# Kernel tuning notes

Hardware: AMD Instinct MI355X
Metric: run time of the kernel (lower is better)

Reference implementation:

```python
import jax, jax.numpy as jnp
import numpy as np

N, R, A, F = 6000, 5, 8, 128
K, O = 2, 128
RADIUS = 0.028
ROT_DELTA = 1


def _kernel_matrix(n_radial, n_angular, radius):
    # polar grid of kernel vertices -> cartesian, shape (R, A, 2)
    r = radius * (np.arange(1, n_radial + 1, dtype=np.float64) / n_radial)
    theta = 2.0 * np.pi * np.arange(n_angular, dtype=np.float64) / n_angular
    x = r[:, None] * np.cos(theta)[None, :]
    y = r[:, None] * np.sin(theta)[None, :]
    return np.stack([x, y], axis=-1)


def _interp_coefficients(n_radial, n_angular, radius):
    # Gaussian interpolation weights w(rho_a,theta_b,rho_c,theta_d), normalized,
    # reshaped to (R, A, R*A) as in _configure_patch_operator.
    kv = _kernel_matrix(n_radial, n_angular, radius)           # (R, A, 2)
    flat = kv.reshape(-1, 2)                                   # (R*A, 2)
    d2 = ((kv[:, :, None, :] - flat[None, None, :, :]) ** 2).sum(-1)  # (R, A, R*A)
    sigma = radius / n_radial
    w = np.exp(-d2 / (2.0 * sigma * sigma))
    w = w / w.sum(axis=-1, keepdims=True)
    return w.astype(np.float32)


def setup_inputs() -> dict:
    key = jax.random.key(0)
    k1, k2, k3, k4, k5 = jax.random.split(key, 5)
    mesh_signal = jax.random.normal(k1, (N, F), dtype=jnp.float32)
    # barycentric coords: channel 0 = vertex indices (stored as float), channel 1 = weights summing to 1
    idx = jax.random.randint(k2, (N, R, A, 3), 0, N).astype(jnp.float32)
    w = jax.random.uniform(k3, (N, R, A, 3), dtype=jnp.float32)
    w = w / w.sum(axis=-1, keepdims=True)
    bary_coordinates = jnp.stack([idx, w], axis=-1)            # (N, R, A, 3, 2)
    kernel_weights = jax.random.normal(k4, (R, A, K, O, F), dtype=jnp.float32) * 0.05
    bias = jax.random.normal(k5, (K, O), dtype=jnp.float32) * 0.05
    interp_coeffs = jnp.asarray(_interp_coefficients(R, A, RADIUS))  # (R, A, R*A)
    return {"mesh_signal": mesh_signal, "bary_coordinates": bary_coordinates,
            "kernel_weights": kernel_weights, "bias": bias, "interp_coeffs": interp_coeffs}


def reference(mesh_signal, bary_coordinates, kernel_weights, bias, interp_coeffs):
    # 1) gather + barycentric interpolation
    idx = bary_coordinates[..., 0].astype(jnp.int32)           # (N, R, A, 3)
    w = bary_coordinates[..., 1]                               # (N, R, A, 3)
    collected = mesh_signal[idx]                               # (N, R, A, 3, F)
    sig = jnp.sum(w[..., None] * collected, axis=-2)           # (N, R, A, F)
    # 2) patch operator: F_x @ I[a,b]
    flat = sig.reshape(-1, R * A, F)                           # (N, R*A, F)
    patched = jnp.einsum('nqf,raq->nraf', flat, interp_coeffs)  # (N, R, A, F)
    # 3) rotation-shifted fold (splits=1 -> single chunk; splits don't change math)
    outs = []
    for rot in range(0, A, ROT_DELTA):
        rolled = jnp.roll(patched, shift=rot, axis=2)          # (N, R, A, F)
        s = jnp.einsum('nraf,rakof->nko', rolled, kernel_weights) + (R * A) * bias  # (N, K, O)
        outs.append(jax.nn.relu(s).sum(axis=1))                # (N, O)
    return jnp.stack(outs, axis=1)                             # (N, n_rotations, O)
```

## Files before the change

### kernel.cpp

```cpp
#include <hip/hip_runtime.h>
#include <hip/hip_bf16.h>


#define N_PTS 6000
#define RR 5
#define AA 8
#define FF 128
#define OO 128
#define QQ 40
#define KD2 1280
#define SIG_BLOCKS 750
#define W2_BLOCKS 128
#define CCQ 0.70710678118654752f
#define RT2 1.41421356237309515f

#define AHS ((size_t)N_PTS * KD2)
#define BHS ((size_t)512 * KD2)

typedef __bf16 bf16_t;
typedef __bf16 bf16x2 __attribute__((ext_vector_type(2)));
typedef __bf16 bf16x8 __attribute__((ext_vector_type(8)));
typedef float f32x4 __attribute__((ext_vector_type(4)));

#define GLOAD_LDS16(g, l)                                              \
  __builtin_amdgcn_global_load_lds(                                    \
      (const __attribute__((address_space(1))) void*)(g),              \
      (__attribute__((address_space(3))) void*)(l), 16, 0, 0)

#define DFT8V(xx, c, X0, X4, Xr1, Xi1, Xr2, Xi2, Xr3, Xi3)             \
  {                                                                    \
    const float s0_ = xx[0][c] + xx[4][c], s1_ = xx[1][c] + xx[5][c];  \
    const float s2_ = xx[2][c] + xx[6][c], s3_ = xx[3][c] + xx[7][c];  \
    const float d0_ = xx[0][c] - xx[4][c], d1_ = xx[1][c] - xx[5][c];  \
    const float d2_ = xx[2][c] - xx[6][c], d3_ = xx[3][c] - xx[7][c];  \
    const float e_ = CCQ * (d1_ - d3_), o_ = CCQ * (d1_ + d3_);        \
    X0 = (s0_ + s2_) + (s1_ + s3_);                                    \
    X4 = (s0_ + s2_) - (s1_ + s3_);                                    \
    Xr2 = s0_ - s2_; Xi2 = s3_ - s1_;                                  \
    Xr1 = d0_ + e_;  Xi1 = -(o_ + d2_);                                \
    Xr3 = d0_ - e_;  Xi3 = d2_ - o_;                                   \
  }

#define PACKP(dst, P, Q)                                               \
  {                                                                    \
    bf16x8 pv_;                                                        \
    pv_[0] = (bf16_t)P[0]; pv_[1] = (bf16_t)Q[0];                      \
    pv_[2] = (bf16_t)P[1]; pv_[3] = (bf16_t)Q[1];                      \
    pv_[4] = (bf16_t)P[2]; pv_[5] = (bf16_t)Q[2];                      \
    pv_[6] = (bf16_t)P[3]; pv_[7] = (bf16_t)Q[3];                      \
    *(bf16x8*)(dst) = pv_;                                             \
  }

__global__ __launch_bounds__(256, 6) void prep_fft_kernel(
    const float* __restrict__ mesh, const float* __restrict__ bary,
    const float* __restrict__ kw, const float* __restrict__ interp,
    bf16_t* __restrict__ Ahat, bf16_t* __restrict__ Bhat) {
  __shared__ float sh[1920];
  const int bx = blockIdx.x;
  const int tid = threadIdx.x;

  if (bx < SIG_BLOCKS) {
    const int slot = tid >> 5;
    const int l = tid & 31;
    const int n = bx * 8 + slot;
    const float* bbase = bary + (size_t)bx * 8 * (QQ * 6);
    for (int i = tid; i < 1920; i += 256) sh[i] = bbase[i];
    __syncthreads();
    const float* bp = sh + slot * 240;
    bf16_t* an = Ahat + (size_t)n * KD2 + l * 8;
#pragma unroll
    for (int rho = 0; rho < RR; ++rho) {
      float x[8][4];
#pragma unroll
      for (int a = 0; a < 8; ++a) {
        const float* rec = bp + (rho * 8 + a) * 6;
        const float2 p0 = *(const float2*)(rec);
        const float2 p1 = *(const float2*)(rec + 2);
        const float2 p2 = *(const float2*)(rec + 4);
        const float4 v0 =
            *(const float4*)(mesh + (size_t)((int)p0.x) * FF + l * 4);
        const float4 v1 =
            *(const float4*)(mesh + (size_t)((int)p1.x) * FF + l * 4);
        const float4 v2 =
            *(const float4*)(mesh + (size_t)((int)p2.x) * FF + l * 4);
        x[a][0] = p0.y * v0.x + p1.y * v1.x + p2.y * v2.x;
        x[a][1] = p0.y * v0.y + p1.y * v1.y + p2.y * v2.y;
        x[a][2] = p0.y * v0.z + p1.y * v1.z + p2.y * v2.z;
        x[a][3] = p0.y * v0.w + p1.y * v1.w + p2.y * v2.w;
      }
      float X0[4], X4[4], Xr1[4], Xi1[4], Xr2[4], Xi2[4], Xr3[4], Xi3[4];
#pragma unroll
      for (int c = 0; c < 4; ++c)
        DFT8V(x, c, X0[c], X4[c], Xr1[c], Xi1[c], Xr2[c], Xi2[c], Xr3[c],
              Xi3[c]);
      bf16_t* dst = an + rho * 256;
      PACKP(dst, X0, X4);
      PACKP(dst + AHS, Xr1, Xi1);
      PACKP(dst + 2 * AHS, Xr2, Xi2);
      PACKP(dst + 3 * AHS, Xr3, Xi3);
    }
  } else {
    const int j = (bx - SIG_BLOCKS) * 2 + (tid >> 7);
    const int f = tid & 127;
    for (int i = tid; i < RR * AA * QQ; i += 256) sh[i] = interp[i];
    __syncthreads();
    const int o = (j >> 1) & 127;
    const int k = j & 1;
    float acc[QQ];
#pragma unroll
    for (int q = 0; q < QQ; ++q) acc[q] = 0.f;
    for (int r = 0; r < RR; ++r) {
      for (int a = 0; a < AA; ++a) {
        const float kv =
            kw[((size_t)((r * AA + a) * 2 + k) * OO + o) * FF + f];
        const float4* ip = (const float4*)(sh + (r * AA + a) * QQ);
#pragma unroll
        for (int q4 = 0; q4 < QQ / 4; ++q4) {
          const float4 w4 = ip[q4];
          acc[q4 * 4 + 0] += w4.x * kv;
          acc[q4 * 4 + 1] += w4.y * kv;
          acc[q4 * 4 + 2] += w4.z * kv;
          acc[q4 * 4 + 3] += w4.w * kv;
        }
      }
    }
    const float SC = 0.125f;
    bf16_t* b1p = Bhat + (size_t)j * KD2;
    bf16_t* b2p = Bhat + (size_t)(256 + j) * KD2;
#pragma unroll
    for (int rho = 0; rho < RR; ++rho) {
      float xx[8][1];
#pragma unroll
      for (int a = 0; a < 8; ++a) xx[a][0] = acc[rho * 8 + a];
      float Y0, Y4, Yr1, Yi1, Yr2, Yi2, Yr3, Yi3;
      DFT8V(xx, 0, Y0, Y4, Yr1, Yi1, Yr2, Yi2, Yr3, Yi3);
      const int off = rho * 256 + f * 2;
      bf16x2 w;
      w[0] = (bf16_t)(Y0 * SC);   w[1] = (bf16_t)0.f;
      *(bf16x2*)(b1p + off) = w;
      w[0] = (bf16_t)0.f;         w[1] = (bf16_t)(Y4 * SC);
      *(bf16x2*)(b2p + off) = w;
      w[0] = (bf16_t)(Yr1 * SC);  w[1] = (bf16_t)(Yi1 * SC);
      *(bf16x2*)(b1p + BHS + off) = w;
      w[0] = (bf16_t)(Yi1 * SC);  w[1] = (bf16_t)(-Yr1 * SC);
      *(bf16x2*)(b2p + BHS + off) = w;
      w[0] = (bf16_t)(Yr2 * SC);  w[1] = (bf16_t)(Yi2 * SC);
      *(bf16x2*)(b1p + 2 * BHS + off) = w;
      w[0] = (bf16_t)(Yi2 * SC);  w[1] = (bf16_t)(-Yr2 * SC);
      *(bf16x2*)(b2p + 2 * BHS + off) = w;
      w[0] = (bf16_t)(Yr3 * SC);  w[1] = (bf16_t)(Yi3 * SC);
      *(bf16x2*)(b1p + 3 * BHS + off) = w;
      w[0] = (bf16_t)(Yi3 * SC);  w[1] = (bf16_t)(-Yr3 * SC);
      *(bf16x2*)(b2p + 3 * BHS + off) = w;
    }
  }
}

__global__ __launch_bounds__(256, 3) void gemm_fused_fft_kernel(
    const bf16_t* __restrict__ Ahat, const bf16_t* __restrict__ Bhat,
    const float* __restrict__ bias, float* __restrict__ out) {
  const int L = blockIdx.x;
  const int xcd = L & 7;
  const int t = L >> 3;
  const int g = xcd + 8 * (t >> 4);
  const int jt = t & 15;
  const int m0 = g * 128;
  if (m0 >= N_PTS) return;
  const int j0 = jt * 16;

  __shared__ bf16_t As0[128 * 64];
  __shared__ bf16_t As1[128 * 64];
  __shared__ bf16_t Bs0[32 * 64];
  __shared__ bf16_t Bs1[32 * 64];
  const int tid = threadIdx.x;
  const int wave = tid >> 6;
  const int lane = tid & 63;
  const int quad = lane >> 4;
  const int tl = lane & 15;
  const int wm = wave * 32;
  const int srow = lane >> 3;
  const int sc = (lane & 7) ^ srow;

  const int crow = wave * 8;
  const int colbase = (crow < 16) ? (j0 + crow) : (256 + j0 + (crow - 16));
  const int gcol = colbase + srow;

  static const float CF[4][8] = {
      {1, 1, 1, 1, 1, 1, 1, 1},
      {2, RT2, 0, -RT2, -2, -RT2, 0, RT2},
      {2, 0, -2, 0, 2, 0, -2, 0},
      {2, -RT2, 0, RT2, -2, RT2, 0, -RT2}};
  static const float SF[4][8] = {
      {1, -1, 1, -1, 1, -1, 1, -1},
      {0, -RT2, -2, -RT2, 0, RT2, 2, RT2},
      {0, -2, 0, 2, 0, -2, 0, 2},
      {0, -RT2, 2, -RT2, 0, RT2, -2, RT2}};

  f32x4 oacc[8][2];
#pragma unroll
  for (int rot = 0; rot < 8; ++rot)
#pragma unroll
    for (int mm = 0; mm < 2; ++mm) oacc[rot][mm] = {0.f, 0.f, 0.f, 0.f};

#define STAGE_HALF(Asx, Bsx, kkv)                                      \
  {                                                                    \
    _Pragma("unroll") for (int i = 0; i < 4; ++i) {                    \
      const int row = wave * 32 + i * 8;                               \
      int gm = m0 + row + srow;                                        \
      gm = gm < N_PTS ? gm : (N_PTS - 1);                              \
      GLOAD_LDS16(A + (size_t)gm * KD2 + (kkv) + sc * 8,               \
                  Asx + row * 64);                                     \
    }                                                                  \
    GLOAD_LDS16(B + (size_t)gcol * KD2 + (kkv) + sc * 8,               \
                Bsx + crow * 64);                                      \
  }

#define COMPUTE_HALF(Asx, Bsx)                                         \
  {                                                                    \
    _Pragma("unroll") for (int ks = 0; ks < 2; ++ks) {                 \
      const int ch = (((ks * 4 + quad) ^ (tl & 7)) * 8);               \
      bf16x8 af[2], bfr[2];                                            \
      af[0] = *(const bf16x8*)(Asx + (wm + tl) * 64 + ch);             \
      af[1] = *(const bf16x8*)(Asx + (wm + 16 + tl) * 64 + ch);        \
      bfr[0] = *(const bf16x8*)(Bsx + tl * 64 + ch);                   \
      bfr[1] = *(const bf16x8*)(Bsx + (16 + tl) * 64 + ch);            \
      _Pragma("unroll") for (int mm = 0; mm < 2; ++mm)                 \
        _Pragma("unroll") for (int cc = 0; cc < 2; ++cc)               \
          z[mm][cc] = __builtin_amdgcn_mfma_f32_16x16x32_bf16(         \
              af[mm], bfr[cc], z[mm][cc], 0, 0, 0);                    \
    }                                                                  \
  }

#pragma unroll
  for (int b = 0; b < 4; ++b) {
    const bf16_t* A = Ahat + (size_t)b * AHS;
    const bf16_t* B = Bhat + (size_t)b * BHS;
    f32x4 z[2][2];
#pragma unroll
    for (int mm = 0; mm < 2; ++mm)
#pragma unroll
      for (int cc = 0; cc < 2; ++cc) z[mm][cc] = {0.f, 0.f, 0.f, 0.f};

    for (int kk = 0; kk < KD2; kk += 128) {
      __syncthreads();
      STAGE_HALF(As0, Bs0, kk);
      STAGE_HALF(As1, Bs1, kk + 64);
      __syncthreads();
      COMPUTE_HALF(As0, Bs0);
      COMPUTE_HALF(As1, Bs1);
    }
#pragma unroll
    for (int rot = 0; rot < 8; ++rot) {
      const float cf = CF[b][rot], sf = SF[b][rot];
#pragma unroll
      for (int mm = 0; mm < 2; ++mm)
#pragma unroll
        for (int r = 0; r < 4; ++r)
          oacc[rot][mm][r] += cf * z[mm][0][r] + sf * z[mm][1][r];
    }
  }

  const int j = j0 + tl;
  const float bb = 40.0f * bias[((j & 1) << 7) | (j >> 1)];
  const int o = j >> 1;
#pragma unroll
  for (int rot = 0; rot < 8; ++rot)
#pragma unroll
    for (int mm = 0; mm < 2; ++mm)
#pragma unroll
      for (int r = 0; r < 4; ++r) {
        const int mrow = m0 + wm + mm * 16 + quad * 4 + r;
        float v = oacc[rot][mm][r] + bb;
        v = v > 0.f ? v : 0.f;
        const float vs = v + __shfl_xor(v, 1, 64);
        if (((lane & 1) == 0) && (mrow < N_PTS))
          out[(size_t)mrow * 1024 + rot * 128 + o] = vs;
      }
}

extern "C" void kernel_launch(void* const* d_in, const int* in_sizes, int n_in,
                              void* d_out, int out_size, void* d_ws,
                              size_t ws_size, hipStream_t stream) {
  const float* mesh = (const float*)d_in[0];
  const float* bary = (const float*)d_in[1];
  const float* kw = (const float*)d_in[2];
  const float* bias = (const float*)d_in[3];
  const float* interp = (const float*)d_in[4];
  float* out = (float*)d_out;

  bf16_t* Ahat = (bf16_t*)d_ws;
  bf16_t* Bhat = (bf16_t*)((char*)d_ws + 4 * AHS * 2);

  prep_fft_kernel<<<SIG_BLOCKS + W2_BLOCKS, 256, 0, stream>>>(
      mesh, bary, kw, interp, Ahat, Bhat);
  gemm_fused_fft_kernel<<<768, 256, 0, stream>>>(Ahat, Bhat, bias, out);
}
```

Measured before the change: 173.0 us.

## Double-buffer GEMM staging to overlap loads with MFMA, add nontemporal memory hints

Restructures the GEMM K-loop into a software pipeline. The next 64-wide K slice is staged into the alternate LDS buffer while MFMAs run on the current one, and the first slice of the next FFT bin is prefetched across the bin boundary. The aim is to hide global-to-LDS latency that the old stage-all-then-compute loop exposed. Separately, it adds nontemporal hints to the streaming loads and stores in the prep kernel and the output write. The risk is that the async LDS loads may not be complete at the barrier, and the nontemporal hints may hurt reuse of the Ahat intermediates in L2.

```diff
diff --git a/kernel.cpp b/kernel.cpp
--- a/kernel.cpp
+++ b/kernel.cpp
@@ -48,7 +48,7 @@
     pv_[2] = (bf16_t)P[1]; pv_[3] = (bf16_t)Q[1];                      \
     pv_[4] = (bf16_t)P[2]; pv_[5] = (bf16_t)Q[2];                      \
     pv_[6] = (bf16_t)P[3]; pv_[7] = (bf16_t)Q[3];                      \
-    *(bf16x8*)(dst) = pv_;                                             \
+    __builtin_nontemporal_store(pv_, (bf16x8*)(dst));                  \
   }
 
 __global__ __launch_bounds__(256, 6) void prep_fft_kernel(
@@ -64,7 +64,8 @@
     const int l = tid & 31;
     const int n = bx * 8 + slot;
     const float* bbase = bary + (size_t)bx * 8 * (QQ * 6);
-    for (int i = tid; i < 1920; i += 256) sh[i] = bbase[i];
+    for (int i = tid; i < 1920; i += 256)
+      sh[i] = __builtin_nontemporal_load(bbase + i);
     __syncthreads();
     const float* bp = sh + slot * 240;
     bf16_t* an = Ahat + (size_t)n * KD2 + l * 8;
@@ -111,8 +112,8 @@
     for (int q = 0; q < QQ; ++q) acc[q] = 0.f;
     for (int r = 0; r < RR; ++r) {
       for (int a = 0; a < AA; ++a) {
-        const float kv =
-            kw[((size_t)((r * AA + a) * 2 + k) * OO + o) * FF + f];
+        const float kv = __builtin_nontemporal_load(
+            &kw[((size_t)((r * AA + a) * 2 + k) * OO + o) * FF + f]);
         const float4* ip = (const float4*)(sh + (r * AA + a) * QQ);
 #pragma unroll
         for (int q4 = 0; q4 < QQ / 4; ++q4) {
@@ -202,16 +203,16 @@
 #pragma unroll
     for (int mm = 0; mm < 2; ++mm) oacc[rot][mm] = {0.f, 0.f, 0.f, 0.f};
 
-#define STAGE_HALF(Asx, Bsx, kkv)                                      \
+#define STAGE_HALF(Asx, Bsx, Ap, Bp, kkv)                              \
   {                                                                    \
     _Pragma("unroll") for (int i = 0; i < 4; ++i) {                    \
       const int row = wave * 32 + i * 8;                               \
       int gm = m0 + row + srow;                                        \
       gm = gm < N_PTS ? gm : (N_PTS - 1);                              \
-      GLOAD_LDS16(A + (size_t)gm * KD2 + (kkv) + sc * 8,               \
+      GLOAD_LDS16((Ap) + (size_t)gm * KD2 + (kkv) + sc * 8,            \
                   Asx + row * 64);                                     \
     }                                                                  \
-    GLOAD_LDS16(B + (size_t)gcol * KD2 + (kkv) + sc * 8,               \
+    GLOAD_LDS16((Bp) + (size_t)gcol * KD2 + (kkv) + sc * 8,            \
                 Bsx + crow * 64);                                      \
   }
 
@@ -231,6 +232,9 @@
     }                                                                  \
   }
 
+  STAGE_HALF(As0, Bs0, Ahat, Bhat, 0);
+  __syncthreads();
+
 #pragma unroll
   for (int b = 0; b < 4; ++b) {
     const bf16_t* A = Ahat + (size_t)b * AHS;
@@ -241,14 +245,25 @@
 #pragma unroll
       for (int cc = 0; cc < 2; ++cc) z[mm][cc] = {0.f, 0.f, 0.f, 0.f};
 
-    for (int kk = 0; kk < KD2; kk += 128) {
+    int kk = 0;
+#pragma unroll 1
+    for (int d = 0; d < 9; ++d) {
+      STAGE_HALF(As1, Bs1, A, B, kk + 64);
+      COMPUTE_HALF(As0, Bs0);
       __syncthreads();
-      STAGE_HALF(As0, Bs0, kk);
-      STAGE_HALF(As1, Bs1, kk + 64);
+      STAGE_HALF(As0, Bs0, A, B, kk + 128);
+      COMPUTE_HALF(As1, Bs1);
       __syncthreads();
-      COMPUTE_HALF(As0, Bs0);
-      COMPUTE_HALF(As1, Bs1);
-    }
+      kk += 128;
+    }
+    STAGE_HALF(As1, Bs1, A, B, 1216);
+    COMPUTE_HALF(As0, Bs0);
+    __syncthreads();
+    if (b < 3) {
+      STAGE_HALF(As0, Bs0, A + AHS, B + BHS, 0);
+    }
+    COMPUTE_HALF(As1, Bs1);
+    __syncthreads();
 #pragma unroll
     for (int rot = 0; rot < 8; ++rot) {
       const float cf = CF[b][rot], sf = SF[b][rot];
@@ -274,7 +289,8 @@
         v = v > 0.f ? v : 0.f;
         const float vs = v + __shfl_xor(v, 1, 64);
         if (((lane & 1) == 0) && (mrow < N_PTS))
-          out[(size_t)mrow * 1024 + rot * 128 + o] = vs;
+          __builtin_nontemporal_store(
+              vs, &out[(size_t)mrow * 1024 + rot * 128 + o]);
       }
 }
 
```

New measurement: 201.0 us. 1.16x slower.
